# Kernel tuning notes

Measured on AMD Instinct MI355X. Metric: run time of the kernel, lower is better.

Reference implementation:

```python
import jax, jax.numpy as jnp
import numpy as np

_EPS = 1e-8
TEMPERATURE = 0.1  # head_cfg.temperature
WEIGHT = 1.0       # float(head_cfg.weight[1:]) with weight='w1'
N = 100000
K = 31   # nsample - 1
C = 64
NUM_CLASSES = 17


def setup_inputs() -> dict:
    key = jax.random.key(0)
    k1, k2, k3 = jax.random.split(key, 3)
    features = jax.random.normal(k1, (N, C), dtype=jnp.float32)
    labels = jax.random.randint(k2, (N,), 0, NUM_CLASSES, dtype=jnp.int32)
    # KNN neighbor indices with self excluded (original drops idx[...,1:]);
    # offset trick guarantees neighbor_idx[i, j] != i.
    off = jax.random.randint(k3, (N, K), 1, N, dtype=jnp.int32)
    neighbor_idx = (jnp.arange(N, dtype=jnp.int32)[:, None] + off) % N
    return {"features": features, "labels": labels, "neighbor_idx": neighbor_idx}


def reference(features, labels, neighbor_idx):
    # posmask_cnt: argmax of one-hot labels == integer class-id comparison
    neighbor_label = labels[neighbor_idx]                      # (N, K) int
    posmask = labels[:, None] == neighbor_label                # (N, K) bool
    cnt = posmask.sum(axis=1)
    point_mask = (cnt > 0) & (cnt < K)                          # (N,) bool

    # dist_l2 on gathered neighbor features
    neighbor_feature = features[neighbor_idx]                  # (N, K, C)
    diff = features[:, None, :] - neighbor_feature             # (N, K, C)
    dist = jnp.sqrt(jnp.sum(diff * diff, axis=-1)) + _EPS      # (N, K)

    # contrast_softnn
    logits = -dist
    logits = logits - jnp.max(logits, axis=1, keepdims=True)
    logits = logits / TEMPERATURE
    exp = jnp.exp(logits)                                      # (N, K)
    pos = jnp.sum(exp * posmask, axis=1)
    neg = jnp.sum(exp, axis=1)
    loss = -jnp.log(pos / neg + _EPS)                          # (N,)

    # masked mean == torch.mean(loss[point_mask])
    pm = point_mask.astype(loss.dtype)
    denom = jnp.maximum(jnp.sum(pm), 1.0)
    return jnp.sum(loss * pm) / denom * WEIGHT
```

## Files before the change

kernel.cpp:

```cpp
#include <hip/hip_runtime.h>
#include <hip/hip_fp16.h>

#define KNB 31
#define CH 64
#define TEMP_INV 10.0f


__global__ void ch_init_ws(double* __restrict__ ws) {
    ws[0] = 0.0;
    ws[1] = 0.0;
}

__global__ __launch_bounds__(256) void ch_cvt(
    const float* __restrict__ in, __half* __restrict__ out, int total8)
{
    const int idx = blockIdx.x * blockDim.x + threadIdx.x;
    if (idx >= total8) return;
    const float4* ip = reinterpret_cast<const float4*>(in) + (size_t)idx * 2;
    const float4 a = ip[0];
    const float4 b = ip[1];
    union { uint4 u; __half2 h[4]; } o;
    o.h[0] = __floats2half2_rn(a.x, a.y);
    o.h[1] = __floats2half2_rn(a.z, a.w);
    o.h[2] = __floats2half2_rn(b.x, b.y);
    o.h[3] = __floats2half2_rn(b.z, b.w);
    reinterpret_cast<uint4*>(out)[idx] = o.u;
}

template <bool FP16>
__global__ __launch_bounds__(256) void ch_main4(
    const float*  __restrict__ feat,
    const __half* __restrict__ tab,
    const int*    __restrict__ labels,
    const int*    __restrict__ nidx,
    double*       __restrict__ ws,
    int n)
{
    const int t   = threadIdx.x;
    const int i   = blockIdx.x * (256 / 4) + (t >> 2);
    const int sub = t & 3;

    float loss_w = 0.0f;
    float pm_f   = 0.0f;

    if (i < n) {
        float f[16];
        if constexpr (FP16) {
            union { uint4 u[2]; __half2 h[8]; } a;
            const uint4* ap = reinterpret_cast<const uint4*>(tab + (size_t)i * CH + sub * 16);
            a.u[0] = ap[0];
            a.u[1] = ap[1];
            #pragma unroll
            for (int q = 0; q < 8; ++q) {
                const float2 v = __half22float2(a.h[q]);
                f[2 * q]     = v.x;
                f[2 * q + 1] = v.y;
            }
        } else {
            const float4* ap = reinterpret_cast<const float4*>(feat + (size_t)i * CH + sub * 16);
            #pragma unroll
            for (int q = 0; q < 4; ++q) {
                const float4 v = ap[q];
                f[4 * q]     = v.x;
                f[4 * q + 1] = v.y;
                f[4 * q + 2] = v.z;
                f[4 * q + 3] = v.w;
            }
        }

        const int lab = labels[i];

        float m  = -1e30f;
        float se = 0.0f;
        float sp = 0.0f;
        int   cnt = 0;

        #pragma unroll 2
        for (int j = 0; j < KNB; ++j) {
            const int nj = nidx[(size_t)i * KNB + j];

            float s = 0.0f;
            if constexpr (FP16) {
                union { uint4 u[2]; __half2 h[8]; } b;
                const uint4* bp = reinterpret_cast<const uint4*>(tab + (size_t)nj * CH + sub * 16);
                b.u[0] = bp[0];
                b.u[1] = bp[1];
                #pragma unroll
                for (int q = 0; q < 8; ++q) {
                    const float2 v = __half22float2(b.h[q]);
                    const float dx = f[2 * q]     - v.x;
                    const float dy = f[2 * q + 1] - v.y;
                    s += dx * dx + dy * dy;
                }
            } else {
                const float4* bp = reinterpret_cast<const float4*>(feat + (size_t)nj * CH + sub * 16);
                #pragma unroll
                for (int q = 0; q < 4; ++q) {
                    const float4 v = bp[q];
                    const float dx = f[4 * q]     - v.x;
                    const float dy = f[4 * q + 1] - v.y;
                    const float dz = f[4 * q + 2] - v.z;
                    const float dw = f[4 * q + 3] - v.w;
                    s += dx * dx + dy * dy + dz * dz + dw * dw;
                }
            }
            s += __shfl_xor(s, 1);
            s += __shfl_xor(s, 2);

            const float dist = sqrtf(s) + 1e-8f;
            const float l = -dist;

            const bool pm = (labels[nj] == lab);
            cnt += pm ? 1 : 0;

            if (l > m) {
                const float r = __expf((m - l) * TEMP_INV);
                se *= r;
                sp *= r;
                m = l;
            }
            const float e = __expf((l - m) * TEMP_INV);
            se += e;
            if (pm) sp += e;
        }

        if (sub == 0 && cnt > 0 && cnt < KNB) {
            loss_w = -logf(sp / se + 1e-8f);
            pm_f   = 1.0f;
        }
    }

    __shared__ float s_l[256];
    __shared__ float s_c[256];
    s_l[t] = loss_w;
    s_c[t] = pm_f;
    __syncthreads();
    #pragma unroll
    for (int off = 128; off > 0; off >>= 1) {
        if (t < off) {
            s_l[t] += s_l[t + off];
            s_c[t] += s_c[t + off];
        }
        __syncthreads();
    }
    if (t == 0) {
        atomicAdd(ws,     (double)s_l[0]);
        atomicAdd(ws + 1, (double)s_c[0]);
    }
}

__global__ void ch_finalize(const double* __restrict__ ws, float* __restrict__ out) {
    double c = ws[1];
    if (c < 1.0) c = 1.0;
    out[0] = (float)(ws[0] / c);
}

extern "C" void kernel_launch(void* const* d_in, const int* in_sizes, int n_in,
                              void* d_out, int out_size, void* d_ws, size_t ws_size,
                              hipStream_t stream) {
    const float* feat   = (const float*)d_in[0];
    const int*   labels = (const int*)d_in[1];
    const int*   nidx   = (const int*)d_in[2];
    float*       out    = (float*)d_out;
    double*      ws     = (double*)d_ws;

    const int n = in_sizes[1];
    const size_t tab_bytes = (size_t)n * CH * sizeof(__half);
    const bool fp16_ok = ws_size >= 256 + tab_bytes;

    ch_init_ws<<<1, 1, 0, stream>>>(ws);

    const int blocks = (n + 63) / 64;
    if (fp16_ok) {
        __half* tab = reinterpret_cast<__half*>((char*)d_ws + 256);
        const int total8 = n * CH / 8;
        ch_cvt<<<(total8 + 255) / 256, 256, 0, stream>>>(feat, tab, total8);
        ch_main4<true><<<blocks, 256, 0, stream>>>(feat, tab, labels, nidx, ws, n);
    } else {
        ch_main4<false><<<blocks, 256, 0, stream>>>(feat, nullptr, labels, nidx, ws, n);
    }

    ch_finalize<<<1, 1, 0, stream>>>(ws, out);
}
```

Measured before the change: 93.51 us.

## Use 8 lanes per point, batch neighbor loads, two-pass softmax, fp16 dot2

Each point is now handled by 8 lanes with 8 channels each instead of 4 lanes with 16, giving more threads in flight for the gather-bound loads. All 31 neighbor indices and labels are loaded up front and the loop is fully unrolled, so many independent gathers can be outstanding at once. The online-softmax rescaling is replaced by a min-then-sum two-pass over a register array. Squared distances in the fp16 path are computed with packed half subtraction and the fdot2 builtin. The fp16 differences are rounded to half precision before squaring, and register pressure rises from the unrolled arrays.

```diff
diff --git a/kernel.cpp b/kernel.cpp
--- a/kernel.cpp
+++ b/kernel.cpp
@@ -4,6 +4,8 @@
 #define KNB 31
 #define CH 64
 #define TEMP_INV 10.0f
+
+typedef _Float16 h2 __attribute__((ext_vector_type(2)));
 
 
 __global__ void ch_init_ws(double* __restrict__ ws) {
@@ -27,8 +29,17 @@
     reinterpret_cast<uint4*>(out)[idx] = o.u;
 }
 
+__device__ __forceinline__ float dot2acc(h2 d, float s) {
+#if defined(__has_builtin) && __has_builtin(__builtin_amdgcn_fdot2)
+    return __builtin_amdgcn_fdot2(d, d, s, false);
+#else
+    const float x = (float)d[0], y = (float)d[1];
+    return s + x * x + y * y;
+#endif
+}
+
 template <bool FP16>
-__global__ __launch_bounds__(256) void ch_main4(
+__global__ __launch_bounds__(256) void ch_main8(
     const float*  __restrict__ feat,
     const __half* __restrict__ tab,
     const int*    __restrict__ labels,
@@ -37,93 +48,80 @@
     int n)
 {
     const int t   = threadIdx.x;
-    const int i   = blockIdx.x * (256 / 4) + (t >> 2);
-    const int sub = t & 3;
+    const int i   = blockIdx.x * (256 / 8) + (t >> 3);
+    const int sub = t & 7;
 
     float loss_w = 0.0f;
     float pm_f   = 0.0f;
 
     if (i < n) {
-        float f[16];
+        union { uint4 u; h2 h[4]; } A;
+        float af[8];
         if constexpr (FP16) {
-            union { uint4 u[2]; __half2 h[8]; } a;
-            const uint4* ap = reinterpret_cast<const uint4*>(tab + (size_t)i * CH + sub * 16);
-            a.u[0] = ap[0];
-            a.u[1] = ap[1];
-            #pragma unroll
-            for (int q = 0; q < 8; ++q) {
-                const float2 v = __half22float2(a.h[q]);
-                f[2 * q]     = v.x;
-                f[2 * q + 1] = v.y;
-            }
+            A.u = *reinterpret_cast<const uint4*>(tab + (size_t)i * CH + sub * 8);
         } else {
-            const float4* ap = reinterpret_cast<const float4*>(feat + (size_t)i * CH + sub * 16);
-            #pragma unroll
-            for (int q = 0; q < 4; ++q) {
-                const float4 v = ap[q];
-                f[4 * q]     = v.x;
-                f[4 * q + 1] = v.y;
-                f[4 * q + 2] = v.z;
-                f[4 * q + 3] = v.w;
-            }
+            const float4* ap = reinterpret_cast<const float4*>(feat + (size_t)i * CH + sub * 8);
+            const float4 v0 = ap[0], v1 = ap[1];
+            af[0] = v0.x; af[1] = v0.y; af[2] = v0.z; af[3] = v0.w;
+            af[4] = v1.x; af[5] = v1.y; af[6] = v1.z; af[7] = v1.w;
         }
 
         const int lab = labels[i];
 
-        float m  = -1e30f;
-        float se = 0.0f;
-        float sp = 0.0f;
-        int   cnt = 0;
+        int nj[KNB];
+        #pragma unroll
+        for (int j = 0; j < KNB; ++j)
+            nj[j] = nidx[(size_t)i * KNB + j];
 
-        #pragma unroll 2
+        unsigned pmask = 0u;
+        #pragma unroll
+        for (int j = 0; j < KNB; ++j)
+            pmask |= (labels[nj[j]] == lab) ? (1u << j) : 0u;
+
+        float dist[KNB];
+        #pragma unroll
         for (int j = 0; j < KNB; ++j) {
-            const int nj = nidx[(size_t)i * KNB + j];
-
             float s = 0.0f;
             if constexpr (FP16) {
-                union { uint4 u[2]; __half2 h[8]; } b;
-                const uint4* bp = reinterpret_cast<const uint4*>(tab + (size_t)nj * CH + sub * 16);
-                b.u[0] = bp[0];
-                b.u[1] = bp[1];
+                union { uint4 u; h2 h[4]; } B;
+                B.u = *reinterpret_cast<const uint4*>(tab + (size_t)nj[j] * CH + sub * 8);
                 #pragma unroll
-                for (int q = 0; q < 8; ++q) {
-                    const float2 v = __half22float2(b.h[q]);
-                    const float dx = f[2 * q]     - v.x;
-                    const float dy = f[2 * q + 1] - v.y;
-                    s += dx * dx + dy * dy;
+                for (int q = 0; q < 4; ++q) {
+                    const h2 d = A.h[q] - B.h[q];
+                    s = dot2acc(d, s);
                 }
             } else {
-                const float4* bp = reinterpret_cast<const float4*>(feat + (size_t)nj * CH + sub * 16);
-                #pragma unroll
-                for (int q = 0; q < 4; ++q) {
-                    const float4 v = bp[q];
-                    const float dx = f[4 * q]     - v.x;
-                    const float dy = f[4 * q + 1] - v.y;
-                    const float dz = f[4 * q + 2] - v.z;
-                    const float dw = f[4 * q + 3] - v.w;
-                    s += dx * dx + dy * dy + dz * dz + dw * dw;
-                }
+                const float4* bp = reinterpret_cast<const float4*>(feat + (size_t)nj[j] * CH + sub * 8);
+                const float4 v0 = bp[0], v1 = bp[1];
+                float d;
+                d = af[0] - v0.x; s += d * d;
+                d = af[1] - v0.y; s += d * d;
+                d = af[2] - v0.z; s += d * d;
+                d = af[3] - v0.w; s += d * d;
+                d = af[4] - v1.x; s += d * d;
+                d = af[5] - v1.y; s += d * d;
+                d = af[6] - v1.z; s += d * d;
+                d = af[7] - v1.w; s += d * d;
             }
             s += __shfl_xor(s, 1);
             s += __shfl_xor(s, 2);
-
-            const float dist = sqrtf(s) + 1e-8f;
-            const float l = -dist;
-
-            const bool pm = (labels[nj] == lab);
-            cnt += pm ? 1 : 0;
-
-            if (l > m) {
-                const float r = __expf((m - l) * TEMP_INV);
-                se *= r;
-                sp *= r;
-                m = l;
-            }
-            const float e = __expf((l - m) * TEMP_INV);
-            se += e;
-            if (pm) sp += e;
+            s += __shfl_xor(s, 4);
+            dist[j] = sqrtf(s) + 1e-8f;
         }
 
+        float mn = dist[0];
+        #pragma unroll
+        for (int j = 1; j < KNB; ++j) mn = fminf(mn, dist[j]);
+
+        float se = 0.0f, sp = 0.0f;
+        #pragma unroll
+        for (int j = 0; j < KNB; ++j) {
+            const float e = __expf((mn - dist[j]) * TEMP_INV);
+            se += e;
+            sp += ((pmask >> j) & 1u) ? e : 0.0f;
+        }
+
+        const int cnt = __popc(pmask);
         if (sub == 0 && cnt > 0 && cnt < KNB) {
             loss_w = -logf(sp / se + 1e-8f);
             pm_f   = 1.0f;
@@ -170,14 +168,14 @@
 
     ch_init_ws<<<1, 1, 0, stream>>>(ws);
 
-    const int blocks = (n + 63) / 64;
+    const int blocks = (n + 31) / 32;
     if (fp16_ok) {
         __half* tab = reinterpret_cast<__half*>((char*)d_ws + 256);
         const int total8 = n * CH / 8;
         ch_cvt<<<(total8 + 255) / 256, 256, 0, stream>>>(feat, tab, total8);
-        ch_main4<true><<<blocks, 256, 0, stream>>>(feat, tab, labels, nidx, ws, n);
+        ch_main8<true><<<blocks, 256, 0, stream>>>(feat, tab, labels, nidx, ws, n);
     } else {
-        ch_main4<false><<<blocks, 256, 0, stream>>>(feat, nullptr, labels, nidx, ws, n);
+        ch_main8<false><<<blocks, 256, 0, stream>>>(feat, nullptr, labels, nidx, ws, n);
     }
 
     ch_finalize<<<1, 1, 0, stream>>>(ws, out);
```

After: 113.2 us. 1.21x slower.

## Assign one neighbor per lane with fp16 dot2 distances and two-pass softmax

Applied to the files above, without the earlier changes.

Restructures the fp16 main kernel so that eight lanes share a point and each lane handles whole neighbors (j = g*8+sub), rather than four lanes splitting the 64 channels of every neighbor. Distances are computed with packed half subtraction and the fdot2 builtin. The online max-rescale softmax becomes a lane-local min followed by shuffle reductions of the exp sums, with the positive mask gathered as a bitmask. The workspace init is folded into the conversion kernel to save one launch. In exchange, the half-precision subtraction changes numerics, each lane issues its own scattered row gathers, and the uint4 A[8] row held per lane adds register pressure.

```diff
diff --git a/kernel.cpp b/kernel.cpp
--- a/kernel.cpp
+++ b/kernel.cpp
@@ -5,6 +5,8 @@
 #define CH 64
 #define TEMP_INV 10.0f
 
+typedef _Float16 h2 __attribute__((ext_vector_type(2)));
+
 
 __global__ void ch_init_ws(double* __restrict__ ws) {
     ws[0] = 0.0;
@@ -12,9 +14,14 @@
 }
 
 __global__ __launch_bounds__(256) void ch_cvt(
-    const float* __restrict__ in, __half* __restrict__ out, int total8)
+    const float* __restrict__ in, __half* __restrict__ out,
+    double* __restrict__ ws, int total8)
 {
     const int idx = blockIdx.x * blockDim.x + threadIdx.x;
+    if (idx == 0) {
+        ws[0] = 0.0;
+        ws[1] = 0.0;
+    }
     if (idx >= total8) return;
     const float4* ip = reinterpret_cast<const float4*>(in) + (size_t)idx * 2;
     const float4 a = ip[0];
@@ -27,9 +34,16 @@
     reinterpret_cast<uint4*>(out)[idx] = o.u;
 }
 
-template <bool FP16>
-__global__ __launch_bounds__(256) void ch_main4(
-    const float*  __restrict__ feat,
+__device__ __forceinline__ float dot2acc(h2 d, float s) {
+#if defined(__has_builtin) && __has_builtin(__builtin_amdgcn_fdot2)
+    return __builtin_amdgcn_fdot2(d, d, s, false);
+#else
+    const float x = (float)d[0], y = (float)d[1];
+    return s + x * x + y * y;
+#endif
+}
+
+__global__ __launch_bounds__(256, 4) void ch_mainT(
     const __half* __restrict__ tab,
     const int*    __restrict__ labels,
     const int*    __restrict__ nidx,
@@ -37,93 +51,74 @@
     int n)
 {
     const int t   = threadIdx.x;
-    const int i   = blockIdx.x * (256 / 4) + (t >> 2);
-    const int sub = t & 3;
+    const int i   = blockIdx.x * (256 / 8) + (t >> 3);
+    const int sub = t & 7;
 
     float loss_w = 0.0f;
     float pm_f   = 0.0f;
 
     if (i < n) {
-        float f[16];
-        if constexpr (FP16) {
-            union { uint4 u[2]; __half2 h[8]; } a;
-            const uint4* ap = reinterpret_cast<const uint4*>(tab + (size_t)i * CH + sub * 16);
-            a.u[0] = ap[0];
-            a.u[1] = ap[1];
+        const uint4* ap = reinterpret_cast<const uint4*>(tab + (size_t)i * CH);
+        uint4 A[8];
+        #pragma unroll
+        for (int q = 0; q < 8; ++q) A[q] = ap[q];
+
+        const int lab = labels[i];
+
+        unsigned mymask = 0u;
+        float dloc[4];
+
+        #pragma unroll
+        for (int g = 0; g < 4; ++g) {
+            const int j     = g * 8 + sub;
+            const bool valid = (j < KNB);
+            const int jc    = valid ? j : (KNB - 1);
+            const int nj    = nidx[(size_t)i * KNB + jc];
+
+            const uint4* bp = reinterpret_cast<const uint4*>(tab + (size_t)nj * CH);
+            float s = 0.0f;
             #pragma unroll
             for (int q = 0; q < 8; ++q) {
-                const float2 v = __half22float2(a.h[q]);
-                f[2 * q]     = v.x;
-                f[2 * q + 1] = v.y;
-            }
-        } else {
-            const float4* ap = reinterpret_cast<const float4*>(feat + (size_t)i * CH + sub * 16);
-            #pragma unroll
-            for (int q = 0; q < 4; ++q) {
-                const float4 v = ap[q];
-                f[4 * q]     = v.x;
-                f[4 * q + 1] = v.y;
-                f[4 * q + 2] = v.z;
-                f[4 * q + 3] = v.w;
-            }
-        }
-
-        const int lab = labels[i];
-
-        float m  = -1e30f;
-        float se = 0.0f;
-        float sp = 0.0f;
-        int   cnt = 0;
-
-        #pragma unroll 2
-        for (int j = 0; j < KNB; ++j) {
-            const int nj = nidx[(size_t)i * KNB + j];
-
-            float s = 0.0f;
-            if constexpr (FP16) {
-                union { uint4 u[2]; __half2 h[8]; } b;
-                const uint4* bp = reinterpret_cast<const uint4*>(tab + (size_t)nj * CH + sub * 16);
-                b.u[0] = bp[0];
-                b.u[1] = bp[1];
+                union { uint4 u; h2 h[4]; } Bv, Av;
+                Bv.u = bp[q];
+                Av.u = A[q];
                 #pragma unroll
-                for (int q = 0; q < 8; ++q) {
-                    const float2 v = __half22float2(b.h[q]);
-                    const float dx = f[2 * q]     - v.x;
-                    const float dy = f[2 * q + 1] - v.y;
-                    s += dx * dx + dy * dy;
-                }
-            } else {
-                const float4* bp = reinterpret_cast<const float4*>(feat + (size_t)nj * CH + sub * 16);
-                #pragma unroll
-                for (int q = 0; q < 4; ++q) {
-                    const float4 v = bp[q];
-                    const float dx = f[4 * q]     - v.x;
-                    const float dy = f[4 * q + 1] - v.y;
-                    const float dz = f[4 * q + 2] - v.z;
-                    const float dw = f[4 * q + 3] - v.w;
-                    s += dx * dx + dy * dy + dz * dz + dw * dw;
+                for (int k = 0; k < 4; ++k) {
+                    const h2 d = Av.h[k] - Bv.h[k];
+                    s = dot2acc(d, s);
                 }
             }
-            s += __shfl_xor(s, 1);
-            s += __shfl_xor(s, 2);
-
-            const float dist = sqrtf(s) + 1e-8f;
-            const float l = -dist;
-
-            const bool pm = (labels[nj] == lab);
-            cnt += pm ? 1 : 0;
-
-            if (l > m) {
-                const float r = __expf((m - l) * TEMP_INV);
-                se *= r;
-                sp *= r;
-                m = l;
-            }
-            const float e = __expf((l - m) * TEMP_INV);
+
+            const bool pm = valid && (labels[nj] == lab);
+            mymask |= pm ? (1u << jc) : 0u;
+            dloc[g] = valid ? (sqrtf(s) + 1e-8f) : 1e30f;
+        }
+
+        mymask |= __shfl_xor((int)mymask, 1);
+        mymask |= __shfl_xor((int)mymask, 2);
+        mymask |= __shfl_xor((int)mymask, 4);
+
+        float mn = fminf(fminf(dloc[0], dloc[1]), fminf(dloc[2], dloc[3]));
+        mn = fminf(mn, __shfl_xor(mn, 1));
+        mn = fminf(mn, __shfl_xor(mn, 2));
+        mn = fminf(mn, __shfl_xor(mn, 4));
+
+        float se = 0.0f, sp = 0.0f;
+        #pragma unroll
+        for (int g = 0; g < 4; ++g) {
+            const int j = g * 8 + sub;
+            const float e = (j < KNB) ? __expf((mn - dloc[g]) * TEMP_INV) : 0.0f;
             se += e;
-            if (pm) sp += e;
-        }
-
+            sp += ((mymask >> (j & 31)) & 1u) ? e : 0.0f;
+        }
+        se += __shfl_xor(se, 1);
+        se += __shfl_xor(se, 2);
+        se += __shfl_xor(se, 4);
+        sp += __shfl_xor(sp, 1);
+        sp += __shfl_xor(sp, 2);
+        sp += __shfl_xor(sp, 4);
+
+        const int cnt = __popc(mymask);
         if (sub == 0 && cnt > 0 && cnt < KNB) {
             loss_w = -logf(sp / se + 1e-8f);
             pm_f   = 1.0f;
@@ -149,6 +144,82 @@
     }
 }
 
+__global__ __launch_bounds__(256) void ch_main4f(
+    const float* __restrict__ feat,
+    const int*   __restrict__ labels,
+    const int*   __restrict__ nidx,
+    double*      __restrict__ ws,
+    int n)
+{
+    const int t   = threadIdx.x;
+    const int i   = blockIdx.x * (256 / 4) + (t >> 2);
+    const int sub = t & 3;
+
+    float loss_w = 0.0f;
+    float pm_f   = 0.0f;
+
+    if (i < n) {
+        float f[16];
+        const float4* ap = reinterpret_cast<const float4*>(feat + (size_t)i * CH + sub * 16);
+        #pragma unroll
+        for (int q = 0; q < 4; ++q) {
+            const float4 v = ap[q];
+            f[4 * q] = v.x; f[4 * q + 1] = v.y; f[4 * q + 2] = v.z; f[4 * q + 3] = v.w;
+        }
+        const int lab = labels[i];
+        float m = -1e30f, se = 0.0f, sp = 0.0f;
+        int cnt = 0;
+        for (int j = 0; j < KNB; ++j) {
+            const int nj = nidx[(size_t)i * KNB + j];
+            const float4* bp = reinterpret_cast<const float4*>(feat + (size_t)nj * CH + sub * 16);
+            float s = 0.0f;
+            #pragma unroll
+            for (int q = 0; q < 4; ++q) {
+                const float4 v = bp[q];
+                float d;
+                d = f[4 * q]     - v.x; s += d * d;
+                d = f[4 * q + 1] - v.y; s += d * d;
+                d = f[4 * q + 2] - v.z; s += d * d;
+                d = f[4 * q + 3] - v.w; s += d * d;
+            }
+            s += __shfl_xor(s, 1);
+            s += __shfl_xor(s, 2);
+            const float l = -(sqrtf(s) + 1e-8f);
+            const bool pm = (labels[nj] == lab);
+            cnt += pm ? 1 : 0;
+            if (l > m) {
+                const float r = __expf((m - l) * TEMP_INV);
+                se *= r; sp *= r; m = l;
+            }
+            const float e = __expf((l - m) * TEMP_INV);
+            se += e;
+            if (pm) sp += e;
+        }
+        if (sub == 0 && cnt > 0 && cnt < KNB) {
+            loss_w = -logf(sp / se + 1e-8f);
+            pm_f   = 1.0f;
+        }
+    }
+
+    __shared__ float s_l[256];
+    __shared__ float s_c[256];
+    s_l[t] = loss_w;
+    s_c[t] = pm_f;
+    __syncthreads();
+    #pragma unroll
+    for (int off = 128; off > 0; off >>= 1) {
+        if (t < off) {
+            s_l[t] += s_l[t + off];
+            s_c[t] += s_c[t + off];
+        }
+        __syncthreads();
+    }
+    if (t == 0) {
+        atomicAdd(ws,     (double)s_l[0]);
+        atomicAdd(ws + 1, (double)s_c[0]);
+    }
+}
+
 __global__ void ch_finalize(const double* __restrict__ ws, float* __restrict__ out) {
     double c = ws[1];
     if (c < 1.0) c = 1.0;
@@ -168,16 +239,16 @@
     const size_t tab_bytes = (size_t)n * CH * sizeof(__half);
     const bool fp16_ok = ws_size >= 256 + tab_bytes;
 
-    ch_init_ws<<<1, 1, 0, stream>>>(ws);
-
-    const int blocks = (n + 63) / 64;
     if (fp16_ok) {
         __half* tab = reinterpret_cast<__half*>((char*)d_ws + 256);
         const int total8 = n * CH / 8;
-        ch_cvt<<<(total8 + 255) / 256, 256, 0, stream>>>(feat, tab, total8);
-        ch_main4<true><<<blocks, 256, 0, stream>>>(feat, tab, labels, nidx, ws, n);
+        ch_cvt<<<(total8 + 255) / 256, 256, 0, stream>>>(feat, tab, ws, total8);
+        const int blocks = (n + 31) / 32;
+        ch_mainT<<<blocks, 256, 0, stream>>>(tab, labels, nidx, ws, n);
     } else {
-        ch_main4<false><<<blocks, 256, 0, stream>>>(feat, nullptr, labels, nidx, ws, n);
+        ch_init_ws<<<1, 1, 0, stream>>>(ws);
+        const int blocks = (n + 63) / 64;
+        ch_main4f<<<blocks, 256, 0, stream>>>(feat, labels, nidx, ws, n);
     }
 
     ch_finalize<<<1, 1, 0, stream>>>(ws, out);
```

New measurement: 149.2 us. 1.6x slower.

## Use FP8 feature table and fold init and finalize into other kernels

Applied to the files above, without the earlier changes.

Converts features to an FP8 table instead of FP16 when the builtins exist, which halves the bytes of each random neighbor gather. Workspace zeroing moves into the convert kernel, and the finalize kernel is replaced by a last-block-done counter in the main kernel, cutting launches from four to two. The FP16 path now uses packed half subtraction with a dot2 accumulate. FP8 quantization of features adds sizable error to the distances, which the temperature of 0.1 amplifies, so the result may miss the reference tolerance.

```diff
diff --git a/kernel.cpp b/kernel.cpp
--- a/kernel.cpp
+++ b/kernel.cpp
@@ -5,16 +5,58 @@
 #define CH 64
 #define TEMP_INV 10.0f
 
-
-__global__ void ch_init_ws(double* __restrict__ ws) {
+typedef _Float16 h2 __attribute__((ext_vector_type(2)));
+typedef float f2 __attribute__((ext_vector_type(2)));
+
+#if (__has_builtin(__builtin_amdgcn_cvt_pk_fp8_f32) && __has_builtin(__builtin_amdgcn_cvt_pk_f32_fp8))
+#define HAS_FP8 1
+#else
+#define HAS_FP8 0
+#endif
+
+
+__device__ __forceinline__ float dot2acc(h2 d, float s) {
+#if defined(__has_builtin) && __has_builtin(__builtin_amdgcn_fdot2)
+    return __builtin_amdgcn_fdot2(d, d, s, false);
+#else
+    const float x = (float)d[0], y = (float)d[1];
+    return s + x * x + y * y;
+#endif
+}
+
+__global__ void ch_init_ws(double* __restrict__ ws, unsigned* __restrict__ ctr) {
     ws[0] = 0.0;
     ws[1] = 0.0;
-}
-
-__global__ __launch_bounds__(256) void ch_cvt(
-    const float* __restrict__ in, __half* __restrict__ out, int total8)
+    *ctr  = 0u;
+}
+
+#if HAS_FP8
+__global__ __launch_bounds__(256) void ch_cvt8(
+    const float* __restrict__ in, unsigned char* __restrict__ out,
+    double* __restrict__ ws, unsigned* __restrict__ ctr, int total8)
 {
     const int idx = blockIdx.x * blockDim.x + threadIdx.x;
+    if (idx == 0) { ws[0] = 0.0; ws[1] = 0.0; *ctr = 0u; }
+    if (idx >= total8) return;
+    const float4* ip = reinterpret_cast<const float4*>(in) + (size_t)idx * 2;
+    const float4 a = ip[0];
+    const float4 b = ip[1];
+    unsigned lo = 0u, hi = 0u;
+    lo = __builtin_amdgcn_cvt_pk_fp8_f32(a.x, a.y, lo, false);
+    lo = __builtin_amdgcn_cvt_pk_fp8_f32(a.z, a.w, lo, true);
+    hi = __builtin_amdgcn_cvt_pk_fp8_f32(b.x, b.y, hi, false);
+    hi = __builtin_amdgcn_cvt_pk_fp8_f32(b.z, b.w, hi, true);
+    uint2 o; o.x = lo; o.y = hi;
+    reinterpret_cast<uint2*>(out)[idx] = o;
+}
+#endif
+
+__global__ __launch_bounds__(256) void ch_cvt16(
+    const float* __restrict__ in, __half* __restrict__ out,
+    double* __restrict__ ws, unsigned* __restrict__ ctr, int total8)
+{
+    const int idx = blockIdx.x * blockDim.x + threadIdx.x;
+    if (idx == 0) { ws[0] = 0.0; ws[1] = 0.0; *ctr = 0u; }
     if (idx >= total8) return;
     const float4* ip = reinterpret_cast<const float4*>(in) + (size_t)idx * 2;
     const float4 a = ip[0];
@@ -27,13 +69,16 @@
     reinterpret_cast<uint4*>(out)[idx] = o.u;
 }
 
-template <bool FP16>
-__global__ __launch_bounds__(256) void ch_main4(
-    const float*  __restrict__ feat,
-    const __half* __restrict__ tab,
-    const int*    __restrict__ labels,
-    const int*    __restrict__ nidx,
-    double*       __restrict__ ws,
+template <int MODE>
+__global__ __launch_bounds__(256) void ch_main_o(
+    const unsigned char* __restrict__ tab8,
+    const __half*        __restrict__ tab16,
+    const float*         __restrict__ feat,
+    const int*           __restrict__ labels,
+    const int*           __restrict__ nidx,
+    double*              __restrict__ ws,
+    unsigned*            __restrict__ ctr,
+    float*               __restrict__ out,
     int n)
 {
     const int t   = threadIdx.x;
@@ -44,27 +89,28 @@
     float pm_f   = 0.0f;
 
     if (i < n) {
-        float f[16];
-        if constexpr (FP16) {
-            union { uint4 u[2]; __half2 h[8]; } a;
-            const uint4* ap = reinterpret_cast<const uint4*>(tab + (size_t)i * CH + sub * 16);
-            a.u[0] = ap[0];
-            a.u[1] = ap[1];
+        float fA[16];
+        union { uint4 u[2]; h2 h[8]; } A16;
+        if constexpr (MODE == 0) {
+            union { uint4 u; unsigned w[4]; } Au;
+            Au.u = *(reinterpret_cast<const uint4*>(tab8 + (size_t)i * CH) + sub);
             #pragma unroll
-            for (int q = 0; q < 8; ++q) {
-                const float2 v = __half22float2(a.h[q]);
-                f[2 * q]     = v.x;
-                f[2 * q + 1] = v.y;
-            }
+            for (int q = 0; q < 4; ++q) {
+                const f2 p0 = __builtin_amdgcn_cvt_pk_f32_fp8(Au.w[q], false);
+                const f2 p1 = __builtin_amdgcn_cvt_pk_f32_fp8(Au.w[q], true);
+                fA[4 * q + 0] = p0[0]; fA[4 * q + 1] = p0[1];
+                fA[4 * q + 2] = p1[0]; fA[4 * q + 3] = p1[1];
+            }
+        } else if constexpr (MODE == 1) {
+            const uint4* ap = reinterpret_cast<const uint4*>(tab16 + (size_t)i * CH + sub * 16);
+            A16.u[0] = ap[0];
+            A16.u[1] = ap[1];
         } else {
             const float4* ap = reinterpret_cast<const float4*>(feat + (size_t)i * CH + sub * 16);
             #pragma unroll
             for (int q = 0; q < 4; ++q) {
                 const float4 v = ap[q];
-                f[4 * q]     = v.x;
-                f[4 * q + 1] = v.y;
-                f[4 * q + 2] = v.z;
-                f[4 * q + 3] = v.w;
+                fA[4 * q] = v.x; fA[4 * q + 1] = v.y; fA[4 * q + 2] = v.z; fA[4 * q + 3] = v.w;
             }
         }
 
@@ -80,36 +126,45 @@
             const int nj = nidx[(size_t)i * KNB + j];
 
             float s = 0.0f;
-            if constexpr (FP16) {
-                union { uint4 u[2]; __half2 h[8]; } b;
-                const uint4* bp = reinterpret_cast<const uint4*>(tab + (size_t)nj * CH + sub * 16);
-                b.u[0] = bp[0];
-                b.u[1] = bp[1];
+            if constexpr (MODE == 0) {
+                union { uint4 u; unsigned w[4]; } Bu;
+                Bu.u = *(reinterpret_cast<const uint4*>(tab8 + (size_t)nj * CH) + sub);
+                #pragma unroll
+                for (int q = 0; q < 4; ++q) {
+                    const f2 p0 = __builtin_amdgcn_cvt_pk_f32_fp8(Bu.w[q], false);
+                    const f2 p1 = __builtin_amdgcn_cvt_pk_f32_fp8(Bu.w[q], true);
+                    float d;
+                    d = fA[4 * q + 0] - p0[0]; s = fmaf(d, d, s);
+                    d = fA[4 * q + 1] - p0[1]; s = fmaf(d, d, s);
+                    d = fA[4 * q + 2] - p1[0]; s = fmaf(d, d, s);
+                    d = fA[4 * q + 3] - p1[1]; s = fmaf(d, d, s);
+                }
+            } else if constexpr (MODE == 1) {
+                union { uint4 u[2]; h2 h[8]; } B;
+                const uint4* bp = reinterpret_cast<const uint4*>(tab16 + (size_t)nj * CH + sub * 16);
+                B.u[0] = bp[0];
+                B.u[1] = bp[1];
                 #pragma unroll
                 for (int q = 0; q < 8; ++q) {
-                    const float2 v = __half22float2(b.h[q]);
-                    const float dx = f[2 * q]     - v.x;
-                    const float dy = f[2 * q + 1] - v.y;
-                    s += dx * dx + dy * dy;
+                    const h2 d = A16.h[q] - B.h[q];
+                    s = dot2acc(d, s);
                 }
             } else {
                 const float4* bp = reinterpret_cast<const float4*>(feat + (size_t)nj * CH + sub * 16);
                 #pragma unroll
                 for (int q = 0; q < 4; ++q) {
                     const float4 v = bp[q];
-                    const float dx = f[4 * q]     - v.x;
-                    const float dy = f[4 * q + 1] - v.y;
-                    const float dz = f[4 * q + 2] - v.z;
-                    const float dw = f[4 * q + 3] - v.w;
-                    s += dx * dx + dy * dy + dz * dz + dw * dw;
+                    float d;
+                    d = fA[4 * q]     - v.x; s = fmaf(d, d, s);
+                    d = fA[4 * q + 1] - v.y; s = fmaf(d, d, s);
+                    d = fA[4 * q + 2] - v.z; s = fmaf(d, d, s);
+                    d = fA[4 * q + 3] - v.w; s = fmaf(d, d, s);
                 }
             }
             s += __shfl_xor(s, 1);
             s += __shfl_xor(s, 2);
 
-            const float dist = sqrtf(s) + 1e-8f;
-            const float l = -dist;
-
+            const float l = -(sqrtf(s) + 1e-8f);
             const bool pm = (labels[nj] == lab);
             cnt += pm ? 1 : 0;
 
@@ -146,13 +201,15 @@
     if (t == 0) {
         atomicAdd(ws,     (double)s_l[0]);
         atomicAdd(ws + 1, (double)s_c[0]);
-    }
-}
-
-__global__ void ch_finalize(const double* __restrict__ ws, float* __restrict__ out) {
-    double c = ws[1];
-    if (c < 1.0) c = 1.0;
-    out[0] = (float)(ws[0] / c);
+        __threadfence();
+        const unsigned old = atomicAdd(ctr, 1u);
+        if (old == gridDim.x - 1) {
+            const double sl = atomicAdd(ws, 0.0);
+            const double sc = atomicAdd(ws + 1, 0.0);
+            const double c  = (sc < 1.0) ? 1.0 : sc;
+            out[0] = (float)(sl / c);
+        }
+    }
 }
 
 extern "C" void kernel_launch(void* const* d_in, const int* in_sizes, int n_in,
@@ -163,22 +220,29 @@
     const int*   nidx   = (const int*)d_in[2];
     float*       out    = (float*)d_out;
     double*      ws     = (double*)d_ws;
+    unsigned*    ctr    = (unsigned*)((char*)d_ws + 16);
 
     const int n = in_sizes[1];
-    const size_t tab_bytes = (size_t)n * CH * sizeof(__half);
-    const bool fp16_ok = ws_size >= 256 + tab_bytes;
-
-    ch_init_ws<<<1, 1, 0, stream>>>(ws);
-
+    const int total8 = n * CH / 8;
     const int blocks = (n + 63) / 64;
-    if (fp16_ok) {
+
+#if HAS_FP8
+    if (ws_size >= 256 + (size_t)n * CH) {
+        unsigned char* tab = (unsigned char*)d_ws + 256;
+        ch_cvt8<<<(total8 + 255) / 256, 256, 0, stream>>>(feat, tab, ws, ctr, total8);
+        ch_main_o<0><<<blocks, 256, 0, stream>>>(tab, nullptr, nullptr,
+                                                 labels, nidx, ws, ctr, out, n);
+        return;
+    }
+#endif
+    if (ws_size >= 256 + (size_t)n * CH * 2) {
         __half* tab = reinterpret_cast<__half*>((char*)d_ws + 256);
-        const int total8 = n * CH / 8;
-        ch_cvt<<<(total8 + 255) / 256, 256, 0, stream>>>(feat, tab, total8);
-        ch_main4<true><<<blocks, 256, 0, stream>>>(feat, tab, labels, nidx, ws, n);
+        ch_cvt16<<<(total8 + 255) / 256, 256, 0, stream>>>(feat, tab, ws, ctr, total8);
+        ch_main_o<1><<<blocks, 256, 0, stream>>>(nullptr, tab, nullptr,
+                                                 labels, nidx, ws, ctr, out, n);
     } else {
-        ch_main4<false><<<blocks, 256, 0, stream>>>(feat, nullptr, labels, nidx, ws, n);
-    }
-
-    ch_finalize<<<1, 1, 0, stream>>>(ws, out);
-}
+        ch_init_ws<<<1, 1, 0, stream>>>(ws, ctr);
+        ch_main_o<2><<<blocks, 256, 0, stream>>>(nullptr, nullptr, feat,
+                                                 labels, nidx, ws, ctr, out, n);
+    }
+}
```

Result: slower. 123.1 us (+31.7%).
